# Kernel tuning notes

Hardware: AMD Instinct MI355X
Metric: run time of the kernel (lower is better)

## Reference

```python
import jax, jax.numpy as jnp
import numpy as np

N_LAYER = 6
EPS = 1e-5
THETA = 2.0 ** 16


def _ln(x):
    # LayerNorm without affine params, eps=1e-5 (torch default)
    m = x.mean(-1, keepdims=True)
    v = ((x - m) ** 2).mean(-1, keepdims=True)
    return (x - m) * jax.lax.rsqrt(v + EPS)


def _rope(phases, v):
    # rotate-half over interleaved pairs, phases are in cycles (mod 1 -> radians)
    v_rot = jnp.stack([-v[..., 1::2], v[..., ::2]], axis=-1).reshape(v.shape)
    ph = (phases % 1.0) * (2.0 * jnp.pi)
    return v * jnp.cos(ph) + v_rot * jnp.sin(ph)


def _forward(x, conv_w, conv_b, pos_embed, encoder, encoder_v, decoder, freqs, head_w, head_b):
    B, Cin, H, W = x.shape
    nh, D, N = encoder.shape
    P = conv_w.shape[-1]
    hp, wp = H // P, W // P
    T = hp * wp
    # patch embed: Conv2d(k=P, s=P) == unfold + matmul
    xp = x.reshape(B, Cin, hp, P, wp, P)
    tokens = jnp.einsum('bchpwq,dcpq->bhwd', xp, conv_w).reshape(B, T, D) + conv_b
    h = tokens + pos_embed  # (B, T, D); the unit head dim is handled by einsum broadcasting
    phases = jnp.arange(T, dtype=jnp.float32).reshape(1, 1, T, 1) * freqs  # (1,1,T,N)
    scale = 1.0 / jnp.sqrt(jnp.asarray(N, dtype=x.dtype))
    for _ in range(N_LAYER):  # weights are SHARED across layers, as in the module
        hn = _ln(h)  # (B, T, D)
        x_sparse = jax.nn.relu(jnp.einsum('btd,hdn->bhtn', hn, encoder))  # (B,nh,T,N)
        qr = _rope(phases, x_sparse)
        scores = jax.nn.softmax(jnp.einsum('bhtn,bhsn->bhts', qr, qr) * scale, axis=-1)
        yKV = _ln(jnp.einsum('bhts,bsd->bhtd', scores, hn))  # V = ln'd x, broadcast over heads
        y_sparse = jax.nn.relu(jnp.einsum('bhtd,hdn->bhtn', yKV, encoder_v))
        xy_sparse = x_sparse * y_sparse  # (B,nh,T,N)
        z = xy_sparse.transpose(0, 2, 1, 3).reshape(B, T, nh * N)  # (B,T,nh*N), head-major flatten
        yMLP = _ln(z @ decoder)  # (B,T,D)
        h = _ln(hn + yMLP)
    pooled = _ln(h.mean(axis=1))  # (B,D)
    return pooled @ head_w.T + head_b


def setup_inputs():
    key = jax.random.key(0)
    B, Cin, H, P = 64, 3, 224, 16
    D, nh, mult, ncls = 768, 12, 8, 1000
    N = mult * D // nh  # 512
    T = (H // P) ** 2  # 196
    ks = jax.random.split(key, 7)

    def xav(k, shape, fan_in, fan_out):
        a = (6.0 / (fan_in + fan_out)) ** 0.5
        return jax.random.uniform(k, shape, jnp.float32, -a, a)

    x = jax.random.normal(ks[0], (B, Cin, H, H), jnp.float32)
    conv_w = xav(ks[1], (D, Cin, P, P), Cin * P * P, D)
    conv_b = jnp.zeros((D,), jnp.float32)
    pos_embed = jax.random.normal(ks[2], (1, T, D), jnp.float32) * 0.02
    encoder = xav(ks[3], (nh, D, N), D, N)
    encoder_v = xav(ks[4], (nh, D, N), D, N)
    decoder = xav(ks[5], (nh * N, D), nh * N, D)
    i = jnp.arange(N, dtype=jnp.float32)
    freqs = ((1.0 / THETA) ** ((i // 2) * 2.0 / N)).reshape(1, 1, 1, N)  # paired RoPE freqs
    head_w = xav(ks[6], (ncls, D), D, ncls)
    head_b = jnp.zeros((ncls,), jnp.float32)
    return dict(x=x, conv_w=conv_w, conv_b=conv_b, pos_embed=pos_embed,
                encoder=encoder, encoder_v=encoder_v, decoder=decoder,
                freqs=freqs, head_w=head_w, head_b=head_b)


def reference(x, conv_w, conv_b, pos_embed, encoder, encoder_v, decoder, freqs, head_w, head_b):
    return _forward(x, conv_w, conv_b, pos_embed, encoder, encoder_v, decoder, freqs, head_w, head_b)
```

## Files before the change

### kernel.cpp

```cpp
#include <hip/hip_runtime.h>
#include <hip/hip_bf16.h>


typedef short bf16x8 __attribute__((ext_vector_type(8)));
typedef float f32x4 __attribute__((ext_vector_type(4)));
typedef unsigned short u16;

#define LN_EPS 1e-5f
#define SM_SCALE 0.044194173824159216f
#define TWO_PI 6.283185307179586f
#define MC 3136

typedef __attribute__((address_space(3))) unsigned char* as3p;
typedef const __attribute__((address_space(1))) unsigned char* as1p;

__device__ __forceinline__ void gload16(const u16* g, u16* l) {
    __builtin_amdgcn_global_load_lds((as1p)(const void*)g, (as3p)(void*)l, 16, 0, 0);
}

__device__ __forceinline__ u16 f2bf(float f) {
    __hip_bfloat16 h = __float2bfloat16(f);
    return *reinterpret_cast<u16*>(&h);
}
__device__ __forceinline__ float bf2f(u16 u) {
    return __uint_as_float(((unsigned)u) << 16);
}

__device__ __forceinline__ float block_reduce_sum(float v, float* sm) {
    #pragma unroll
    for (int o = 32; o; o >>= 1) v += __shfl_xor(v, o);
    if ((threadIdx.x & 63) == 0) sm[threadIdx.x >> 6] = v;
    __syncthreads();
    float r = sm[0] + sm[1] + sm[2] + sm[3];
    __syncthreads();
    return r;
}

__device__ __forceinline__ void gemm_core64(const u16* __restrict__ A, int lda,
                                            const u16* __restrict__ Bt, int ldb,
                                            int ksteps, f32x4 acc[4][4],
                                            u16* lds_a, u16* lds_b) {
    const int tid = threadIdx.x;
    const int lane = tid & 63;
    const int wave = tid >> 6;
    const int wr = (wave >> 1) * 64;
    const int wc = (wave & 1) * 64;
    const int lr = lane & 15;
    const int lg = lane >> 4;
    const int rx = lr & 7;
    const int srow = tid >> 3;
    const int gslot = (tid & 7) ^ (srow & 7);
    const u16* ga = A + (long)srow * lda + gslot * 8;
    const u16* gb = Bt + (long)srow * ldb + gslot * 8;
    u16* la = lds_a + tid * 8;
    u16* lb = lds_b + tid * 8;
    for (int k0 = 0; k0 < ksteps; ++k0) {
        __syncthreads();
        #pragma unroll
        for (int j = 0; j < 4; ++j) {
            gload16(ga + (long)(j * 32) * lda, la + j * 2048);
            gload16(gb + (long)(j * 32) * ldb, lb + j * 2048);
        }
        ga += 64; gb += 64;
        __syncthreads();
        bf16x8 af[2][4], bfr[2][4];
        #pragma unroll
        for (int kk = 0; kk < 2; ++kk) {
            const int ps = ((lg + kk * 4) ^ rx) * 8;
            #pragma unroll
            for (int m = 0; m < 4; m++)
                af[kk][m] = *(const bf16x8*)&lds_a[(wr + 16 * m + lr) * 64 + ps];
            #pragma unroll
            for (int n = 0; n < 4; n++)
                bfr[kk][n] = *(const bf16x8*)&lds_b[(wc + 16 * n + lr) * 64 + ps];
        }
        #pragma unroll
        for (int kk = 0; kk < 2; ++kk)
            #pragma unroll
            for (int m = 0; m < 4; m++)
                #pragma unroll
                for (int n = 0; n < 4; n++)
                    acc[m][n] = __builtin_amdgcn_mfma_f32_16x16x32_bf16(
                        af[kk][m], bfr[kk][n], acc[m][n], 0, 0, 0);
    }
}

#define GEMM64_PROLOGUE                                 \
    __shared__ alignas(16) u16 lds_ab[2 * 128 * 64];    \
    u16* lds_a = lds_ab;                                \
    u16* lds_b = lds_ab + 128 * 64;                     \
    f32x4 acc[4][4];                                    \
    _Pragma("unroll")                                   \
    for (int m = 0; m < 4; m++)                         \
        _Pragma("unroll")                               \
        for (int n = 0; n < 4; n++)                     \
            acc[m][n] = (f32x4){0.f, 0.f, 0.f, 0.f};

#define EPI_VARS                                        \
    const int lane = threadIdx.x & 63;                  \
    const int wave = threadIdx.x >> 6;                  \
    const int ewr = (wave >> 1) * 64 + (lane >> 4) * 4; \
    const int ewc = (wave & 1) * 64 + (lane & 15);

__device__ __forceinline__ void gemm_core(const u16* __restrict__ A, int lda,
                                          const u16* __restrict__ Bt, int ldb,
                                          int ksteps, f32x4 acc[4][4],
                                          u16* lds_a, u16* lds_b) {
    const int tid = threadIdx.x;
    const int lane = tid & 63;
    const int wave = tid >> 6;
    const int wr = (wave >> 1) * 64;
    const int wc = (wave & 1) * 64;
    const int lr = lane & 15;
    const int lk = (lane >> 4) * 8;
    const int srow = tid >> 2;
    const int scol = (tid & 3) * 8;
    const u16* ga = A + (long)srow * lda + scol;
    const u16* gb = Bt + (long)srow * ldb + scol;
    const long ha = (long)64 * lda;
    const long hb = (long)64 * ldb;
    u16* la = lds_a + tid * 8;
    u16* lb = lds_b + tid * 8;
    for (int k0 = 0; k0 < ksteps; ++k0) {
        __syncthreads();
        gload16(ga, la);
        gload16(ga + ha, la + 2048);
        gload16(gb, lb);
        gload16(gb + hb, lb + 2048);
        ga += 32; gb += 32;
        __syncthreads();
        bf16x8 af[4], bfr[4];
        #pragma unroll
        for (int m = 0; m < 4; m++)
            af[m] = *(const bf16x8*)&lds_a[(wr + 16 * m + lr) * 32 + lk];
        #pragma unroll
        for (int n = 0; n < 4; n++)
            bfr[n] = *(const bf16x8*)&lds_b[(wc + 16 * n + lr) * 32 + lk];
        #pragma unroll
        for (int m = 0; m < 4; m++)
            #pragma unroll
            for (int n = 0; n < 4; n++)
                acc[m][n] = __builtin_amdgcn_mfma_f32_16x16x32_bf16(af[m], bfr[n], acc[m][n], 0, 0, 0);
    }
}

__global__ __launch_bounds__(256) void k_pack_patches(const float* __restrict__ x,
                                                      u16* __restrict__ ap) {
    int idx = blockIdx.x * 256 + threadIdx.x;
    int r = idx / 768, k = idx - r * 768;
    int b = r / 196, t = r - b * 196;
    int hp = t / 14, wp = t - hp * 14;
    int c = k >> 8, rem = k & 255, p = rem >> 4, q = rem & 15;
    long src = ((long)(b * 3 + c) * 224 + hp * 16 + p) * 224 + wp * 16 + q;
    ap[idx] = f2bf(x[src]);
}

__global__ __launch_bounds__(256) void k_cast(const float* __restrict__ s,
                                              u16* __restrict__ d, int n) {
    int i = blockIdx.x * 256 + threadIdx.x;
    if (i < n) d[i] = f2bf(s[i]);
}

__global__ __launch_bounds__(256) void k_transpose_cast(const float* __restrict__ src,
                                                        u16* __restrict__ dst,
                                                        int R, int C) {
    __shared__ float tile[32][33];
    int c0 = blockIdx.x * 32, r0 = blockIdx.y * 32;
    long base = (long)blockIdx.z * R * C;
    int i = threadIdx.x >> 5, j = threadIdx.x & 31;
    #pragma unroll
    for (int p = 0; p < 4; p++) {
        int rr = i + p * 8;
        tile[rr][j] = src[base + (long)(r0 + rr) * C + c0 + j];
    }
    __syncthreads();
    #pragma unroll
    for (int p = 0; p < 4; p++) {
        int rr = i + p * 8;
        dst[base + (long)(c0 + rr) * R + r0 + j] = f2bf(tile[j][rr]);
    }
}

__global__ __launch_bounds__(256) void k_rope_tab(const float* __restrict__ freqs,
                                                  float* __restrict__ tc,
                                                  float* __restrict__ ts) {
    int idx = blockIdx.x * 256 + threadIdx.x;
    int t = idx >> 9, n = idx & 511;
    float ph = (float)t * freqs[n];
    ph = (ph - floorf(ph)) * TWO_PI;
    tc[idx] = cosf(ph);
    ts[idx] = sinf(ph);
}

__global__ __launch_bounds__(256) void k_colsum(const float* __restrict__ encv,
                                                float* __restrict__ cs) {
    int h = blockIdx.y, c = blockIdx.x * 256 + threadIdx.x;
    const float* base = encv + (long)h * 768 * 512 + c;
    float a = 0.f;
    for (int d = 0; d < 768; d++) a += base[(long)d * 512];
    cs[h * 512 + c] = a;
}

__global__ __launch_bounds__(256) void k_gemm_tokens(const u16* __restrict__ ap,
                                                     const u16* __restrict__ bw,
                                                     const float* __restrict__ cb,
                                                     const float* __restrict__ pe,
                                                     float* __restrict__ hout) {
    GEMM64_PROLOGUE
    int row0 = blockIdx.x * 128, col0 = blockIdx.y * 128;
    gemm_core64(ap + (long)row0 * 768, 768, bw + (long)col0 * 768, 768, 12, acc, lds_a, lds_b);
    EPI_VARS
    const int tid = threadIdx.x;
    float* TF = (float*)lds_ab;
    #pragma unroll
    for (int hf = 0; hf < 2; ++hf) {
        __syncthreads();
        if ((ewr >> 6) == hf) {
            #pragma unroll
            for (int m = 0; m < 4; m++)
                #pragma unroll
                for (int n = 0; n < 4; n++)
                    #pragma unroll
                    for (int i = 0; i < 4; i++) {
                        int row = row0 + ewr + 16 * m + i;
                        int col = col0 + ewc + 16 * n;
                        int t = row % 196;
                        TF[(ewr - hf * 64 + 16 * m + i) * 128 + ewc + 16 * n] =
                            acc[m][n][i] + cb[col] + pe[t * 768 + col];
                    }
        }
        __syncthreads();
        #pragma unroll
        for (int q = 0; q < 8; ++q) {
            int chunk = tid + q * 256;
            int r = chunk >> 5, c = chunk & 31;
            *(f32x4*)&hout[(long)(row0 + hf * 64 + r) * 768 + col0 + c * 4] =
                *(f32x4*)&TF[r * 128 + c * 4];
        }
    }
}

__global__ __launch_bounds__(256) void k_gemm_xs(const u16* __restrict__ hnb,
                                                 const u16* __restrict__ enct,
                                                 const float* __restrict__ tc,
                                                 const float* __restrict__ tsn,
                                                 u16* __restrict__ xs,
                                                 u16* __restrict__ qr) {
    GEMM64_PROLOGUE
    int p = blockIdx.x + 25 * blockIdx.y;
    int w = (p & 7) * 150 + (p >> 3);
    int row0 = (w % 25) * 128, col0 = (w / 25) * 128;
    int head = col0 >> 9, nn0 = col0 & 511;
    gemm_core64(hnb + (long)row0 * 768, 768,
                enct + ((long)head * 512 + nn0) * 768, 768, 12, acc, lds_a, lds_b);
    EPI_VARS
    const int tid = threadIdx.x;
    u16* TU = lds_ab;
    __syncthreads();
    #pragma unroll
    for (int m = 0; m < 4; m++)
        #pragma unroll
        for (int n = 0; n < 4; n++)
            #pragma unroll
            for (int i = 0; i < 4; i++)
                TU[(ewr + 16 * m + i) * 128 + ewc + 16 * n] =
                    f2bf(fmaxf(acc[m][n][i], 0.f));
    __syncthreads();
    #pragma unroll
    for (int q = 0; q < 8; ++q) {
        int chunk = tid + q * 256;
        int r = chunk >> 4, c = chunk & 15;
        int row = row0 + r;
        if (row < MC)
            *(bf16x8*)&xs[((long)head * MC + row) * 512 + nn0 + c * 8] =
                *(bf16x8*)&TU[r * 128 + c * 8];
    }
    __syncthreads();
    #pragma unroll
    for (int m = 0; m < 4; m++)
        #pragma unroll
        for (int n = 0; n < 4; n++)
            #pragma unroll
            for (int i = 0; i < 4; i++) {
                int row = row0 + ewr + 16 * m + i;
                float v = fmaxf(acc[m][n][i], 0.f);
                float pp = __shfl_xor(v, 1);
                if (row < MC) {
                    int t = row % 196;
                    int nn = nn0 + ewc + 16 * n;
                    float cs = tc[t * 512 + nn], sn = tsn[t * 512 + nn];
                    float rot = (nn & 1) ? pp : -pp;
                    TU[(ewr + 16 * m + i) * 128 + ewc + 16 * n] =
                        f2bf(v * cs + rot * sn);
                }
            }
    __syncthreads();
    #pragma unroll
    for (int q = 0; q < 8; ++q) {
        int chunk = tid + q * 256;
        int r = chunk >> 4, c = chunk & 15;
        int row = row0 + r;
        if (row < MC)
            *(bf16x8*)&qr[((long)head * MC + row) * 512 + nn0 + c * 8] =
                *(bf16x8*)&TU[r * 128 + c * 8];
    }
}

__global__ __launch_bounds__(256) void k_attn(const u16* __restrict__ qr,
                                              const u16* __restrict__ hnT,
                                              u16* __restrict__ ykv,
                                              float* __restrict__ stats) {
    __shared__ alignas(16) u16 lds_a[128 * 32];
    __shared__ alignas(16) u16 lds_b[128 * 32];
    __shared__ alignas(16) u16 Pl[128 * 232];
    __shared__ float part[2][128][2];
    const int tid = threadIdx.x, lane = tid & 63, wave = tid >> 6;
    const int wr = (wave >> 1) * 64, wc = (wave & 1) * 64;
    const int lr = lane & 15, lk = (lane >> 4) * 8;
    const int row0 = blockIdx.x * 128, bh = blockIdx.y;
    const int bL = bh & 15;
    const u16* qbase = qr + (long)bh * 196 * 512;

    f32x4 acc0[4][4], acc1[4][4];
    #pragma unroll
    for (int m = 0; m < 4; m++)
        #pragma unroll
        for (int n = 0; n < 4; n++) {
            acc0[m][n] = (f32x4){0.f, 0.f, 0.f, 0.f};
            acc1[m][n] = (f32x4){0.f, 0.f, 0.f, 0.f};
        }
    gemm_core(qbase + (long)row0 * 512, 512, qbase, 512, 16, acc0, lds_a, lds_b);
    gemm_core(qbase + (long)row0 * 512, 512, qbase + 128 * 512, 512, 16, acc1, lds_a, lds_b);

    const int rb = wr + (lane >> 4) * 4;
    #pragma unroll
    for (int m = 0; m < 4; m++)
        #pragma unroll
        for (int i = 0; i < 4; i++) {
            float mx = -1e30f;
            #pragma unroll
            for (int n = 0; n < 4; n++) {
                int c0 = wc + 16 * n + lr;
                if (c0 < 196) mx = fmaxf(mx, acc0[m][n][i]);
                if (c0 + 128 < 196) mx = fmaxf(mx, acc1[m][n][i]);
            }
            #pragma unroll
            for (int o = 1; o < 16; o <<= 1) mx = fmaxf(mx, __shfl_xor(mx, o));
            if (lr == 0) part[0][rb + 16 * m + i][wave & 1] = mx;
        }
    __syncthreads();
    #pragma unroll
    for (int m = 0; m < 4; m++)
        #pragma unroll
        for (int i = 0; i < 4; i++) {
            int row = rb + 16 * m + i;
            float rmx = fmaxf(part[0][row][0], part[0][row][1]);
            float s = 0.f;
            #pragma unroll
            for (int n = 0; n < 4; n++) {
                int c0 = wc + 16 * n + lr;
                float e0 = (c0 < 196) ? __expf((acc0[m][n][i] - rmx) * SM_SCALE) : 0.f;
                float e1 = (c0 + 128 < 196) ? __expf((acc1[m][n][i] - rmx) * SM_SCALE) : 0.f;
                acc0[m][n][i] = e0; acc1[m][n][i] = e1;
                s += e0 + e1;
            }
            #pragma unroll
            for (int o = 1; o < 16; o <<= 1) s += __shfl_xor(s, o);
            if (lr == 0) part[1][row][wave & 1] = s;
        }
    __syncthreads();
    #pragma unroll
    for (int m = 0; m < 4; m++)
        #pragma unroll
        for (int i = 0; i < 4; i++) {
            int row = rb + 16 * m + i;
            float inv = 1.f / (part[1][row][0] + part[1][row][1]);
            #pragma unroll
            for (int n = 0; n < 4; n++) {
                int c0 = wc + 16 * n + lr;
                Pl[row * 232 + c0] = f2bf(acc0[m][n][i] * inv);
                if (c0 + 128 < 224)
                    Pl[row * 232 + c0 + 128] = f2bf(acc1[m][n][i] * inv);
            }
        }
    __syncthreads();
    { float* pf = &part[0][0][0]; pf[tid] = 0.f; pf[tid + 256] = 0.f; }
    const int srow = tid >> 2, scol = (tid & 3) * 8;
    for (int cd = 0; cd < 6; ++cd) {
        const u16* Bt = hnT + ((long)bL * 768 + cd * 128) * 224;
        f32x4 acc[4][4];
        #pragma unroll
        for (int m = 0; m < 4; m++)
            #pragma unroll
            for (int n = 0; n < 4; n++) acc[m][n] = (f32x4){0.f, 0.f, 0.f, 0.f};
        for (int k0 = 0; k0 < 7; ++k0) {
            __syncthreads();
            gload16(Bt + (long)srow * 224 + k0 * 32 + scol, lds_b + tid * 8);
            gload16(Bt + (long)(srow + 64) * 224 + k0 * 32 + scol, lds_b + 2048 + tid * 8);
            __syncthreads();
            bf16x8 af[4], bfr[4];
            #pragma unroll
            for (int m = 0; m < 4; m++)
                af[m] = *(const bf16x8*)&Pl[(wr + 16 * m + lr) * 232 + k0 * 32 + lk];
            #pragma unroll
            for (int n = 0; n < 4; n++)
                bfr[n] = *(const bf16x8*)&lds_b[(wc + 16 * n + lr) * 32 + lk];
            #pragma unroll
            for (int m = 0; m < 4; m++)
                #pragma unroll
                for (int n = 0; n < 4; n++)
                    acc[m][n] = __builtin_amdgcn_mfma_f32_16x16x32_bf16(af[m], bfr[n], acc[m][n], 0, 0, 0);
        }
        #pragma unroll
        for (int m = 0; m < 4; m++)
            #pragma unroll
            for (int i = 0; i < 4; i++) {
                float s = acc[m][0][i] + acc[m][1][i] + acc[m][2][i] + acc[m][3][i];
                float q2 = acc[m][0][i] * acc[m][0][i] + acc[m][1][i] * acc[m][1][i] +
                           acc[m][2][i] * acc[m][2][i] + acc[m][3][i] * acc[m][3][i];
                #pragma unroll
                for (int o = 1; o < 16; o <<= 1) {
                    s += __shfl_xor(s, o);
                    q2 += __shfl_xor(q2, o);
                }
                if (lr == 0) {
                    part[0][rb + 16 * m + i][wave & 1] += s;
                    part[1][rb + 16 * m + i][wave & 1] += q2;
                }
            }
        EPI_VARS
        #pragma unroll
        for (int m = 0; m < 4; m++)
            #pragma unroll
            for (int n = 0; n < 4; n++)
                #pragma unroll
                for (int i = 0; i < 4; i++) {
                    int trow = row0 + ewr + 16 * m + i;
                    if (trow < 196)
                        ykv[((long)bh * 196 + trow) * 768 + cd * 128 + ewc + 16 * n] =
                            f2bf(acc[m][n][i]);
                }
    }
    __syncthreads();
    if (tid < 128) {
        int trow = row0 + tid;
        if (trow < 196) {
            float s = part[0][tid][0] + part[0][tid][1];
            float q2 = part[1][tid][0] + part[1][tid][1];
            float mu = s * (1.f / 768.f);
            float var = q2 * (1.f / 768.f) - mu * mu;
            float2 st;
            st.x = mu;
            st.y = rsqrtf(var + LN_EPS);
            *(float2*)&stats[((long)bh * 196 + trow) * 2] = st;
        }
    }
}

__global__ __launch_bounds__(256) void k_gemm_ys(const u16* __restrict__ ykv,
                                                 const u16* __restrict__ encvt,
                                                 const u16* __restrict__ xs,
                                                 const float* __restrict__ stats,
                                                 const float* __restrict__ colsum,
                                                 u16* __restrict__ z) {
    GEMM64_PROLOGUE
    int p = blockIdx.x + 25 * (blockIdx.y + 4 * blockIdx.z);
    int w = (p & 7) * 150 + (p >> 3);
    int rt = w % 25, rem = w / 25;
    int ct = rem & 3, h = rem >> 2;
    int row0 = rt * 128, col0 = ct * 128;
    gemm_core64(ykv + ((long)h * MC + row0) * 768, 768,
                encvt + ((long)h * 512 + col0) * 768, 768, 12, acc, lds_a, lds_b);
    EPI_VARS
    const int tid = threadIdx.x;
    u16* TU = lds_ab;
    __syncthreads();
    #pragma unroll
    for (int q = 0; q < 8; ++q) {
        int chunk = tid + q * 256;
        int r = chunk >> 4, c = chunk & 15;
        *(bf16x8*)&TU[r * 128 + c * 8] =
            *(const bf16x8*)&xs[((long)h * MC + row0 + r) * 512 + col0 + c * 8];
    }
    __syncthreads();
    #pragma unroll
    for (int m = 0; m < 4; m++)
        #pragma unroll
        for (int i = 0; i < 4; i++) {
            int rloc = ewr + 16 * m + i;
            int row = row0 + rloc;
            float mu = 0.f, rs = 0.f;
            if (row < MC) {
                float2 st = *(const float2*)&stats[((long)h * MC + row) * 2];
                mu = st.x; rs = st.y;
            }
            #pragma unroll
            for (int n = 0; n < 4; n++) {
                int cloc = ewc + 16 * n;
                float cs = colsum[h * 512 + col0 + cloc];
                float v = (acc[m][n][i] - mu * cs) * rs;
                v = fmaxf(v, 0.f) * bf2f(TU[rloc * 128 + cloc]);
                TU[rloc * 128 + cloc] = f2bf(v);
            }
        }
    __syncthreads();
    #pragma unroll
    for (int q = 0; q < 8; ++q) {
        int chunk = tid + q * 256;
        int r = chunk >> 4, c = chunk & 15;
        int row = row0 + r;
        if (row < MC)
            *(bf16x8*)&z[(long)row * 6144 + h * 512 + col0 + c * 8] =
                *(bf16x8*)&TU[r * 128 + c * 8];
    }
}

__global__ __launch_bounds__(256) void k_gemm_mlp(const u16* __restrict__ z,
                                                  const u16* __restrict__ dect,
                                                  float* __restrict__ rawK) {
    GEMM64_PROLOGUE
    int p = blockIdx.x + 25 * (blockIdx.y + 6 * blockIdx.z);
    int w = (p & 7) * 75 + (p >> 3);
    int row0 = (w % 25) * 128, col0 = ((w / 25) % 6) * 128, s = w / 150;
    gemm_core64(z + (long)row0 * 6144 + s * 1536, 6144,
                dect + (long)col0 * 6144 + s * 1536, 6144, 24, acc, lds_a, lds_b);
    EPI_VARS
    const int tid = threadIdx.x;
    float* TF = (float*)lds_ab;
    float* raw = rawK + (long)s * MC * 768;
    #pragma unroll
    for (int hf = 0; hf < 2; ++hf) {
        __syncthreads();
        if ((ewr >> 6) == hf) {
            #pragma unroll
            for (int m = 0; m < 4; m++)
                #pragma unroll
                for (int n = 0; n < 4; n++)
                    #pragma unroll
                    for (int i = 0; i < 4; i++)
                        TF[(ewr - hf * 64 + 16 * m + i) * 128 + ewc + 16 * n] =
                            acc[m][n][i];
        }
        __syncthreads();
        #pragma unroll
        for (int q = 0; q < 8; ++q) {
            int chunk = tid + q * 256;
            int r = chunk >> 5, c = chunk & 31;
            int row = row0 + hf * 64 + r;
            if (row < MC)
                *(f32x4*)&raw[(long)row * 768 + col0 + c * 4] =
                    *(f32x4*)&TF[r * 128 + c * 4];
        }
    }
}

__global__ __launch_bounds__(256) void k_ln1(const float* __restrict__ h,
                                             u16* __restrict__ hnb) {
    __shared__ float sm[4];
    int r = blockIdx.x, tid = threadIdx.x;
    const float* p = h + (long)r * 768;
    float x0 = p[tid], x1 = p[tid + 256], x2 = p[tid + 512];
    float mean = block_reduce_sum(x0 + x1 + x2, sm) * (1.f / 768.f);
    float d0 = x0 - mean, d1 = x1 - mean, d2 = x2 - mean;
    float var = block_reduce_sum(d0 * d0 + d1 * d1 + d2 * d2, sm) * (1.f / 768.f);
    float rs = rsqrtf(var + LN_EPS);
    long ro = (long)r * 768;
    hnb[ro + tid] = f2bf(d0 * rs);
    hnb[ro + tid + 256] = f2bf(d1 * rs);
    hnb[ro + tid + 512] = f2bf(d2 * rs);
}

__global__ __launch_bounds__(256) void k_hnT(const u16* __restrict__ hnb,
                                             u16* __restrict__ hnT) {
    __shared__ u16 tile[32][33];
    int t0 = blockIdx.x * 32, d0 = blockIdx.y * 32, b = blockIdx.z;
    int i = threadIdx.x >> 5, j = threadIdx.x & 31;
    #pragma unroll
    for (int p = 0; p < 4; p++) {
        int t = t0 + i + p * 8;
        tile[i + p * 8][j] = (t < 196) ? hnb[((long)b * 196 + t) * 768 + d0 + j] : (u16)0;
    }
    __syncthreads();
    #pragma unroll
    for (int p = 0; p < 4; p++) {
        int dd = i + p * 8;
        hnT[((long)b * 768 + d0 + dd) * 224 + t0 + j] = tile[j][dd];
    }
}

__global__ __launch_bounds__(256) void k_final_h(const float* __restrict__ rawK,
                                                 u16* __restrict__ hnb) {
    __shared__ float sm[4];
    const long PS = (long)MC * 768;
    int r = blockIdx.x, tid = threadIdx.x;
    const float* rp = rawK + (long)r * 768;
// ... 150 lines not shown
```

Before: 6.880 ms.

## Double-buffer LDS tiles and XOR-swizzle layout in attention kernel GEMMs

Result: slower. 8.286 ms (+20.4%).

```diff
diff --git a/kernel.cpp b/kernel.cpp
--- a/kernel.cpp
+++ b/kernel.cpp
@@ -102,46 +102,55 @@
     const int ewr = (wave >> 1) * 64 + (lane >> 4) * 4; \
     const int ewc = (wave & 1) * 64 + (lane & 15);
 
-__device__ __forceinline__ void gemm_core(const u16* __restrict__ A, int lda,
-                                          const u16* __restrict__ Bt, int ldb,
-                                          int ksteps, f32x4 acc[4][4],
-                                          u16* lds_a, u16* lds_b) {
+__device__ __forceinline__ void gemm_core_sw(const u16* __restrict__ A, int lda,
+                                             const u16* __restrict__ Bt, int ldb,
+                                             int ksteps , f32x4 acc[4][4],
+                                             u16* a0, u16* b0, u16* a1, u16* b1) {
     const int tid = threadIdx.x;
     const int lane = tid & 63;
     const int wave = tid >> 6;
     const int wr = (wave >> 1) * 64;
     const int wc = (wave & 1) * 64;
     const int lr = lane & 15;
-    const int lk = (lane >> 4) * 8;
+    const int lg = lane >> 4;
+    const int ps = (lg ^ ((lr >> 1) & 3)) * 8;
     const int srow = tid >> 2;
-    const int scol = (tid & 3) * 8;
-    const u16* ga = A + (long)srow * lda + scol;
-    const u16* gb = Bt + (long)srow * ldb + scol;
-    const long ha = (long)64 * lda;
-    const long hb = (long)64 * ldb;
-    u16* la = lds_a + tid * 8;
-    u16* lb = lds_b + tid * 8;
-    for (int k0 = 0; k0 < ksteps; ++k0) {
+    const int gslot = (tid & 3) ^ ((srow >> 1) & 3);
+    const u16* ga = A + (long)srow * lda + gslot * 8;
+    const u16* gb = Bt + (long)srow * ldb + gslot * 8;
+    const long ha = (long)64 * lda, hb = (long)64 * ldb;
+
+#define SSTG(pa, pb, k)                                                      \
+    { gload16(ga + (k) * 32, (pa) + tid * 8);                                \
+      gload16(ga + ha + (k) * 32, (pa) + 2048 + tid * 8);                    \
+      gload16(gb + (k) * 32, (pb) + tid * 8);                                \
+      gload16(gb + hb + (k) * 32, (pb) + 2048 + tid * 8); }
+#define SCMP(pa, pb)                                                         \
+    { bf16x8 af[4], bfr[4];                                                  \
+      _Pragma("unroll")                                                      \
+      for (int m = 0; m < 4; m++)                                            \
+          af[m] = *(const bf16x8*)&(pa)[(wr + 16 * m + lr) * 32 + ps];       \
+      _Pragma("unroll")                                                      \
+      for (int n = 0; n < 4; n++)                                            \
+          bfr[n] = *(const bf16x8*)&(pb)[(wc + 16 * n + lr) * 32 + ps];      \
+      _Pragma("unroll")                                                      \
+      for (int m = 0; m < 4; m++)                                            \
+          _Pragma("unroll")                                                  \
+          for (int n = 0; n < 4; n++)                                        \
+              acc[m][n] = __builtin_amdgcn_mfma_f32_16x16x32_bf16(           \
+                  af[m], bfr[n], acc[m][n], 0, 0, 0); }
+
+    SSTG(a0, b0, 0)
+    for (int k0 = 0; k0 < ksteps; k0 += 2) {
         __syncthreads();
-        gload16(ga, la);
-        gload16(ga + ha, la + 2048);
-        gload16(gb, lb);
-        gload16(gb + hb, lb + 2048);
-        ga += 32; gb += 32;
+        if (k0 + 1 < ksteps) SSTG(a1, b1, k0 + 1)
+        SCMP(a0, b0)
         __syncthreads();
-        bf16x8 af[4], bfr[4];
-        #pragma unroll
-        for (int m = 0; m < 4; m++)
-            af[m] = *(const bf16x8*)&lds_a[(wr + 16 * m + lr) * 32 + lk];
-        #pragma unroll
-        for (int n = 0; n < 4; n++)
-            bfr[n] = *(const bf16x8*)&lds_b[(wc + 16 * n + lr) * 32 + lk];
-        #pragma unroll
-        for (int m = 0; m < 4; m++)
-            #pragma unroll
-            for (int n = 0; n < 4; n++)
-                acc[m][n] = __builtin_amdgcn_mfma_f32_16x16x32_bf16(af[m], bfr[n], acc[m][n], 0, 0, 0);
-    }
+        if (k0 + 2 < ksteps) SSTG(a0, b0, k0 + 2)
+        if (k0 + 1 < ksteps) SCMP(a1, b1)
+    }
+#undef SSTG
+#undef SCMP
 }
 
 __global__ __launch_bounds__(256) void k_pack_patches(const float* __restrict__ x,
@@ -316,10 +325,13 @@
     __shared__ float part[2][128][2];
     const int tid = threadIdx.x, lane = tid & 63, wave = tid >> 6;
     const int wr = (wave >> 1) * 64, wc = (wave & 1) * 64;
-    const int lr = lane & 15, lk = (lane >> 4) * 8;
+    const int lr = lane & 15, lg = lane >> 4, lk = lg * 8;
+    const int ps = (lg ^ ((lr >> 1) & 3)) * 8;
     const int row0 = blockIdx.x * 128, bh = blockIdx.y;
     const int bL = bh & 15;
     const u16* qbase = qr + (long)bh * 196 * 512;
+    u16* a1 = Pl;
+    u16* b1 = Pl + 128 * 32;
 
     f32x4 acc0[4][4], acc1[4][4];
     #pragma unroll
@@ -329,8 +341,10 @@
             acc0[m][n] = (f32x4){0.f, 0.f, 0.f, 0.f};
             acc1[m][n] = (f32x4){0.f, 0.f, 0.f, 0.f};
         }
-    gemm_core(qbase + (long)row0 * 512, 512, qbase, 512, 16, acc0, lds_a, lds_b);
-    gemm_core(qbase + (long)row0 * 512, 512, qbase + 128 * 512, 512, 16, acc1, lds_a, lds_b);
+    gemm_core_sw(qbase + (long)row0 * 512, 512, qbase, 512, 16, acc0,
+                 lds_a, lds_b, a1, b1);
+    gemm_core_sw(qbase + (long)row0 * 512, 512, qbase + 128 * 512, 512, 16, acc1,
+                 lds_a, lds_b, a1, b1);
 
     const int rb = wr + (lane >> 4) * 4;
     #pragma unroll
@@ -385,39 +399,51 @@
         }
     __syncthreads();
     { float* pf = &part[0][0][0]; pf[tid] = 0.f; pf[tid + 256] = 0.f; }
-    const int srow = tid >> 2, scol = (tid & 3) * 8;
+    const int srow = tid >> 2;
+    const int gsl = (tid & 3) ^ ((srow >> 1) & 3);
+
+#define PSTG(pb, Btp, k)                                                     \
+    { gload16((Btp) + (long)srow * 224 + (k) * 32 + gsl * 8, (pb) + tid * 8); \
+      gload16((Btp) + (long)(srow + 64) * 224 + (k) * 32 + gsl * 8,          \
+              (pb) + 2048 + tid * 8); }
+#define PCMP(pb, k)                                                          \
+    { bf16x8 af[4], bfr[4];                                                  \
+      _Pragma("unroll")                                                      \
+      for (int m = 0; m < 4; m++)                                            \
+          af[m] = *(const bf16x8*)&Pl[(wr + 16 * m + lr) * 232 + (k) * 32 + lk]; \
+      _Pragma("unroll")                                                      \
+      for (int n = 0; n < 4; n++)                                            \
+          bfr[n] = *(const bf16x8*)&(pb)[(wc + 16 * n + lr) * 32 + ps];      \
+      _Pragma("unroll")                                                      \
+      for (int m = 0; m < 4; m++)                                            \
+          _Pragma("unroll")                                                  \
+          for (int n = 0; n < 4; n++)                                        \
+              pacc[m][n] = __builtin_amdgcn_mfma_f32_16x16x32_bf16(          \
+                  af[m], bfr[n], pacc[m][n], 0, 0, 0); }
+
     for (int cd = 0; cd < 6; ++cd) {
         const u16* Bt = hnT + ((long)bL * 768 + cd * 128) * 224;
-        f32x4 acc[4][4];
+        f32x4 pacc[4][4];
         #pragma unroll
         for (int m = 0; m < 4; m++)
             #pragma unroll
-            for (int n = 0; n < 4; n++) acc[m][n] = (f32x4){0.f, 0.f, 0.f, 0.f};
-        for (int k0 = 0; k0 < 7; ++k0) {
+            for (int n = 0; n < 4; n++) pacc[m][n] = (f32x4){0.f, 0.f, 0.f, 0.f};
+        PSTG(lds_b, Bt, 0)
+        for (int k0 = 0; k0 < 7; k0 += 2) {
             __syncthreads();
-            gload16(Bt + (long)srow * 224 + k0 * 32 + scol, lds_b + tid * 8);
-            gload16(Bt + (long)(srow + 64) * 224 + k0 * 32 + scol, lds_b + 2048 + tid * 8);
+            if (k0 + 1 < 7) PSTG(lds_a, Bt, k0 + 1)
+            PCMP(lds_b, k0)
             __syncthreads();
-            bf16x8 af[4], bfr[4];
-            #pragma unroll
-            for (int m = 0; m < 4; m++)
-                af[m] = *(const bf16x8*)&Pl[(wr + 16 * m + lr) * 232 + k0 * 32 + lk];
-            #pragma unroll
-            for (int n = 0; n < 4; n++)
-                bfr[n] = *(const bf16x8*)&lds_b[(wc + 16 * n + lr) * 32 + lk];
-            #pragma unroll
-            for (int m = 0; m < 4; m++)
-                #pragma unroll
-                for (int n = 0; n < 4; n++)
-                    acc[m][n] = __builtin_amdgcn_mfma_f32_16x16x32_bf16(af[m], bfr[n], acc[m][n], 0, 0, 0);
+            if (k0 + 2 < 7) PSTG(lds_b, Bt, k0 + 2)
+            if (k0 + 1 < 7) PCMP(lds_a, k0 + 1)
         }
         #pragma unroll
         for (int m = 0; m < 4; m++)
             #pragma unroll
             for (int i = 0; i < 4; i++) {
-                float s = acc[m][0][i] + acc[m][1][i] + acc[m][2][i] + acc[m][3][i];
-                float q2 = acc[m][0][i] * acc[m][0][i] + acc[m][1][i] * acc[m][1][i] +
-                           acc[m][2][i] * acc[m][2][i] + acc[m][3][i] * acc[m][3][i];
+                float s = pacc[m][0][i] + pacc[m][1][i] + pacc[m][2][i] + pacc[m][3][i];
+                float q2 = pacc[m][0][i] * pacc[m][0][i] + pacc[m][1][i] * pacc[m][1][i] +
+                           pacc[m][2][i] * pacc[m][2][i] + pacc[m][3][i] * pacc[m][3][i];
                 #pragma unroll
                 for (int o = 1; o < 16; o <<= 1) {
                     s += __shfl_xor(s, o);
@@ -438,9 +464,11 @@
                     int trow = row0 + ewr + 16 * m + i;
                     if (trow < 196)
                         ykv[((long)bh * 196 + trow) * 768 + cd * 128 + ewc + 16 * n] =
-                            f2bf(acc[m][n][i]);
+                            f2bf(pacc[m][n][i]);
                 }
     }
+#undef PSTG
+#undef PCMP
     __syncthreads();
     if (tid < 128) {
         int trow = row0 + tid;
```

## Restructure attention kernel GEMMs with shared A-fragments, wider K-steps and swizzled LDS

Applied to the files above, without the earlier changes.

New measurement: 7.615 ms. +10.7%, slower.

```diff
diff --git a/kernel.cpp b/kernel.cpp
--- a/kernel.cpp
+++ b/kernel.cpp
@@ -102,48 +102,6 @@
     const int ewr = (wave >> 1) * 64 + (lane >> 4) * 4; \
     const int ewc = (wave & 1) * 64 + (lane & 15);
 
-__device__ __forceinline__ void gemm_core(const u16* __restrict__ A, int lda,
-                                          const u16* __restrict__ Bt, int ldb,
-                                          int ksteps, f32x4 acc[4][4],
-                                          u16* lds_a, u16* lds_b) {
-    const int tid = threadIdx.x;
-    const int lane = tid & 63;
-    const int wave = tid >> 6;
-    const int wr = (wave >> 1) * 64;
-    const int wc = (wave & 1) * 64;
-    const int lr = lane & 15;
-    const int lk = (lane >> 4) * 8;
-    const int srow = tid >> 2;
-    const int scol = (tid & 3) * 8;
-    const u16* ga = A + (long)srow * lda + scol;
-    const u16* gb = Bt + (long)srow * ldb + scol;
-    const long ha = (long)64 * lda;
-    const long hb = (long)64 * ldb;
-    u16* la = lds_a + tid * 8;
-    u16* lb = lds_b + tid * 8;
-    for (int k0 = 0; k0 < ksteps; ++k0) {
-        __syncthreads();
-        gload16(ga, la);
-        gload16(ga + ha, la + 2048);
-        gload16(gb, lb);
-        gload16(gb + hb, lb + 2048);
-        ga += 32; gb += 32;
-        __syncthreads();
-        bf16x8 af[4], bfr[4];
-        #pragma unroll
-        for (int m = 0; m < 4; m++)
-            af[m] = *(const bf16x8*)&lds_a[(wr + 16 * m + lr) * 32 + lk];
-        #pragma unroll
-        for (int n = 0; n < 4; n++)
-            bfr[n] = *(const bf16x8*)&lds_b[(wc + 16 * n + lr) * 32 + lk];
-        #pragma unroll
-        for (int m = 0; m < 4; m++)
-            #pragma unroll
-            for (int n = 0; n < 4; n++)
-                acc[m][n] = __builtin_amdgcn_mfma_f32_16x16x32_bf16(af[m], bfr[n], acc[m][n], 0, 0, 0);
-    }
-}
-
 __global__ __launch_bounds__(256) void k_pack_patches(const float* __restrict__ x,
                                                       u16* __restrict__ ap) {
     int idx = blockIdx.x * 256 + threadIdx.x;
@@ -310,16 +268,18 @@
                                               const u16* __restrict__ hnT,
                                               u16* __restrict__ ykv,
                                               float* __restrict__ stats) {
-    __shared__ alignas(16) u16 lds_a[128 * 32];
-    __shared__ alignas(16) u16 lds_b[128 * 32];
+    __shared__ alignas(16) u16 ldsA[128 * 64];
     __shared__ alignas(16) u16 Pl[128 * 232];
     __shared__ float part[2][128][2];
     const int tid = threadIdx.x, lane = tid & 63, wave = tid >> 6;
     const int wr = (wave >> 1) * 64, wc = (wave & 1) * 64;
-    const int lr = lane & 15, lk = (lane >> 4) * 8;
+    const int lr = lane & 15, lg = lane >> 4, lk = lg * 8;
+    const int ewr = wr + lg * 4, ewc = wc + lr;
     const int row0 = blockIdx.x * 128, bh = blockIdx.y;
     const int bL = bh & 15;
     const u16* qbase = qr + (long)bh * 196 * 512;
+    u16* B0 = Pl;
+    u16* B1 = Pl + 128 * 64;
 
     f32x4 acc0[4][4], acc1[4][4];
     #pragma unroll
@@ -329,10 +289,50 @@
             acc0[m][n] = (f32x4){0.f, 0.f, 0.f, 0.f};
             acc1[m][n] = (f32x4){0.f, 0.f, 0.f, 0.f};
         }
-    gemm_core(qbase + (long)row0 * 512, 512, qbase, 512, 16, acc0, lds_a, lds_b);
-    gemm_core(qbase + (long)row0 * 512, 512, qbase + 128 * 512, 512, 16, acc1, lds_a, lds_b);
-
-    const int rb = wr + (lane >> 4) * 4;
+
+    {
+        const int srow = tid >> 3;
+        const int gsl = (tid & 7) ^ (srow & 7);
+        const int rx = lr & 7;
+        const u16* gA = qbase + (long)(row0 + srow) * 512 + gsl * 8;
+        const u16* gB0 = qbase + (long)srow * 512 + gsl * 8;
+        const u16* gB1 = qbase + (long)(128 + srow) * 512 + gsl * 8;
+        for (int k0 = 0; k0 < 8; ++k0) {
+            __syncthreads();
+            #pragma unroll
+            for (int j = 0; j < 4; ++j) {
+                gload16(gA + (long)(32 * j) * 512, ldsA + j * 2048 + tid * 8);
+                gload16(gB0 + (long)(32 * j) * 512, B0 + j * 2048 + tid * 8);
+                gload16(gB1 + (long)(32 * j) * 512, B1 + j * 2048 + tid * 8);
+            }
+            gA += 64; gB0 += 64; gB1 += 64;
+            __syncthreads();
+            #pragma unroll
+            for (int kk = 0; kk < 2; ++kk) {
+                const int ps = ((lg + 4 * kk) ^ rx) * 8;
+                bf16x8 af[4], f0[4], f1[4];
+                #pragma unroll
+                for (int m = 0; m < 4; m++)
+                    af[m] = *(const bf16x8*)&ldsA[(wr + 16 * m + lr) * 64 + ps];
+                #pragma unroll
+                for (int n = 0; n < 4; n++) {
+                    f0[n] = *(const bf16x8*)&B0[(wc + 16 * n + lr) * 64 + ps];
+                    f1[n] = *(const bf16x8*)&B1[(wc + 16 * n + lr) * 64 + ps];
+                }
+                #pragma unroll
+                for (int m = 0; m < 4; m++)
+                    #pragma unroll
+                    for (int n = 0; n < 4; n++) {
+                        acc0[m][n] = __builtin_amdgcn_mfma_f32_16x16x32_bf16(
+                            af[m], f0[n], acc0[m][n], 0, 0, 0);
+                        acc1[m][n] = __builtin_amdgcn_mfma_f32_16x16x32_bf16(
+                            af[m], f1[n], acc1[m][n], 0, 0, 0);
+                    }
+            }
+        }
+    }
+
+    const int rb = wr + lg * 4;
     #pragma unroll
     for (int m = 0; m < 4; m++)
         #pragma unroll
@@ -385,61 +385,82 @@
         }
     __syncthreads();
     { float* pf = &part[0][0][0]; pf[tid] = 0.f; pf[tid + 256] = 0.f; }
-    const int srow = tid >> 2, scol = (tid & 3) * 8;
-    for (int cd = 0; cd < 6; ++cd) {
-        const u16* Bt = hnT + ((long)bL * 768 + cd * 128) * 224;
-        f32x4 acc[4][4];
-        #pragma unroll
-        for (int m = 0; m < 4; m++)
-            #pragma unroll
-            for (int n = 0; n < 4; n++) acc[m][n] = (f32x4){0.f, 0.f, 0.f, 0.f};
-        for (int k0 = 0; k0 < 7; ++k0) {
-            __syncthreads();
-            gload16(Bt + (long)srow * 224 + k0 * 32 + scol, lds_b + tid * 8);
-            gload16(Bt + (long)(srow + 64) * 224 + k0 * 32 + scol, lds_b + 2048 + tid * 8);
-            __syncthreads();
-            bf16x8 af[4], bfr[4];
+
+    {
+        const int srow = tid >> 2;
+        const int gsl = (tid & 3) ^ ((srow >> 1) & 3);
+        const int ps = (lg ^ ((lr >> 1) & 3)) * 8;
+        for (int cp = 0; cp < 3; ++cp) {
+            const u16* Bt0 = hnT + ((long)bL * 768 + (2 * cp) * 128) * 224;
+            const u16* Bt1 = Bt0 + 128 * 224;
+            f32x4 p0[4][4], p1[4][4];
             #pragma unroll
             for (int m = 0; m < 4; m++)
-                af[m] = *(const bf16x8*)&Pl[(wr + 16 * m + lr) * 232 + k0 * 32 + lk];
-            #pragma unroll
-            for (int n = 0; n < 4; n++)
-                bfr[n] = *(const bf16x8*)&lds_b[(wc + 16 * n + lr) * 32 + lk];
+                #pragma unroll
+                for (int n = 0; n < 4; n++) {
+                    p0[m][n] = (f32x4){0.f, 0.f, 0.f, 0.f};
+                    p1[m][n] = (f32x4){0.f, 0.f, 0.f, 0.f};
+                }
+            for (int k0 = 0; k0 < 7; ++k0) {
+                __syncthreads();
+                gload16(Bt0 + (long)srow * 224 + k0 * 32 + gsl * 8, ldsA + tid * 8);
+                gload16(Bt0 + (long)(srow + 64) * 224 + k0 * 32 + gsl * 8, ldsA + 2048 + tid * 8);
+                gload16(Bt1 + (long)srow * 224 + k0 * 32 + gsl * 8, ldsA + 4096 + tid * 8);
+                gload16(Bt1 + (long)(srow + 64) * 224 + k0 * 32 + gsl * 8, ldsA + 6144 + tid * 8);
+                __syncthreads();
+                bf16x8 af[4], f0[4], f1[4];
+                #pragma unroll
+                for (int m = 0; m < 4; m++)
+                    af[m] = *(const bf16x8*)&Pl[(wr + 16 * m + lr) * 232 + k0 * 32 + lk];
+                #pragma unroll
+                for (int n = 0; n < 4; n++) {
+                    f0[n] = *(const bf16x8*)&ldsA[(wc + 16 * n + lr) * 32 + ps];
+                    f1[n] = *(const bf16x8*)&ldsA[4096 + (wc + 16 * n + lr) * 32 + ps];
+                }
+                #pragma unroll
+                for (int m = 0; m < 4; m++)
+                    #pragma unroll
+                    for (int n = 0; n < 4; n++) {
+                        p0[m][n] = __builtin_amdgcn_mfma_f32_16x16x32_bf16(
+                            af[m], f0[n], p0[m][n], 0, 0, 0);
+                        p1[m][n] = __builtin_amdgcn_mfma_f32_16x16x32_bf16(
+                            af[m], f1[n], p1[m][n], 0, 0, 0);
+                    }
+            }
             #pragma unroll
             for (int m = 0; m < 4; m++)
                 #pragma unroll
+                for (int i = 0; i < 4; i++) {
+                    float s = p0[m][0][i] + p0[m][1][i] + p0[m][2][i] + p0[m][3][i]
+                            + p1[m][0][i] + p1[m][1][i] + p1[m][2][i] + p1[m][3][i];
+                    float q2 = p0[m][0][i] * p0[m][0][i] + p0[m][1][i] * p0[m][1][i]
+                             + p0[m][2][i] * p0[m][2][i] + p0[m][3][i] * p0[m][3][i]
+                             + p1[m][0][i] * p1[m][0][i] + p1[m][1][i] * p1[m][1][i]
+                             + p1[m][2][i] * p1[m][2][i] + p1[m][3][i] * p1[m][3][i];
+                    #pragma unroll
+                    for (int o = 1; o < 16; o <<= 1) {
+                        s += __shfl_xor(s, o);
+                        q2 += __shfl_xor(q2, o);
+                    }
+                    if (lr == 0) {
+                        part[0][rb + 16 * m + i][wave & 1] += s;
+                        part[1][rb + 16 * m + i][wave & 1] += q2;
+                    }
+                }
+            #pragma unroll
+            for (int m = 0; m < 4; m++)
+                #pragma unroll
                 for (int n = 0; n < 4; n++)
-                    acc[m][n] = __builtin_amdgcn_mfma_f32_16x16x32_bf16(af[m], bfr[n], acc[m][n], 0, 0, 0);
-        }
-        #pragma unroll
-        for (int m = 0; m < 4; m++)
-            #pragma unroll
-            for (int i = 0; i < 4; i++) {
-                float s = acc[m][0][i] + acc[m][1][i] + acc[m][2][i] + acc[m][3][i];
-                float q2 = acc[m][0][i] * acc[m][0][i] + acc[m][1][i] * acc[m][1][i] +
-                           acc[m][2][i] * acc[m][2][i] + acc[m][3][i] * acc[m][3][i];
-                #pragma unroll
-                for (int o = 1; o < 16; o <<= 1) {
-                    s += __shfl_xor(s, o);
-                    q2 += __shfl_xor(q2, o);
-                }
-                if (lr == 0) {
-                    part[0][rb + 16 * m + i][wave & 1] += s;
-                    part[1][rb + 16 * m + i][wave & 1] += q2;
-                }
-            }
-        EPI_VARS
-        #pragma unroll
-        for (int m = 0; m < 4; m++)
-            #pragma unroll
-            for (int n = 0; n < 4; n++)
-                #pragma unroll
-                for (int i = 0; i < 4; i++) {
-                    int trow = row0 + ewr + 16 * m + i;
-                    if (trow < 196)
-                        ykv[((long)bh * 196 + trow) * 768 + cd * 128 + ewc + 16 * n] =
-                            f2bf(acc[m][n][i]);
-                }
+                    #pragma unroll
+                    for (int i = 0; i < 4; i++) {
+                        int trow = row0 + ewr + 16 * m + i;
+                        if (trow < 196) {
+                            long rbase = ((long)bh * 196 + trow) * 768;
+                            ykv[rbase + (2 * cp) * 128 + ewc + 16 * n] = f2bf(p0[m][n][i]);
+                            ykv[rbase + (2 * cp + 1) * 128 + ewc + 16 * n] = f2bf(p1[m][n][i]);
+                        }
+                    }
+        }
     }
     __syncthreads();
     if (tid < 128) {
```

## Register-prefetch next K tile in GEMM cores and attention, swizzle LDS

Applied to the files above, without the earlier changes.

New measurement: 7.611 ms. +10.6%, slower.

```diff
diff --git a/kernel.cpp b/kernel.cpp
--- a/kernel.cpp
+++ b/kernel.cpp
@@ -10,13 +10,6 @@
 #define SM_SCALE 0.044194173824159216f
 #define TWO_PI 6.283185307179586f
 #define MC 3136
-
-typedef __attribute__((address_space(3))) unsigned char* as3p;
-typedef const __attribute__((address_space(1))) unsigned char* as1p;
-
-__device__ __forceinline__ void gload16(const u16* g, u16* l) {
-    __builtin_amdgcn_global_load_lds((as1p)(const void*)g, (as3p)(void*)l, 16, 0, 0);
-}
 
 __device__ __forceinline__ u16 f2bf(float f) {
     __hip_bfloat16 h = __float2bfloat16(f);
@@ -54,15 +47,28 @@
     const u16* gb = Bt + (long)srow * ldb + gslot * 8;
     u16* la = lds_a + tid * 8;
     u16* lb = lds_b + tid * 8;
+    bf16x8 ra[4], rb[4];
+    #pragma unroll
+    for (int j = 0; j < 4; ++j) {
+        ra[j] = *(const bf16x8*)(ga + (long)(j * 32) * lda);
+        rb[j] = *(const bf16x8*)(gb + (long)(j * 32) * ldb);
+    }
+    ga += 64; gb += 64;
+    #pragma unroll
+    for (int j = 0; j < 4; ++j) {
+        *(bf16x8*)(la + j * 2048) = ra[j];
+        *(bf16x8*)(lb + j * 2048) = rb[j];
+    }
+    __syncthreads();
     for (int k0 = 0; k0 < ksteps; ++k0) {
-        __syncthreads();
-        #pragma unroll
-        for (int j = 0; j < 4; ++j) {
-            gload16(ga + (long)(j * 32) * lda, la + j * 2048);
-            gload16(gb + (long)(j * 32) * ldb, lb + j * 2048);
-        }
-        ga += 64; gb += 64;
-        __syncthreads();
+        if (k0 + 1 < ksteps) {
+            #pragma unroll
+            for (int j = 0; j < 4; ++j) {
+                ra[j] = *(const bf16x8*)(ga + (long)(j * 32) * lda);
+                rb[j] = *(const bf16x8*)(gb + (long)(j * 32) * ldb);
+            }
+            ga += 64; gb += 64;
+        }
         bf16x8 af[2][4], bfr[2][4];
         #pragma unroll
         for (int kk = 0; kk < 2; ++kk) {
@@ -82,6 +88,15 @@
                 for (int n = 0; n < 4; n++)
                     acc[m][n] = __builtin_amdgcn_mfma_f32_16x16x32_bf16(
                         af[kk][m], bfr[kk][n], acc[m][n], 0, 0, 0);
+        __syncthreads();
+        if (k0 + 1 < ksteps) {
+            #pragma unroll
+            for (int j = 0; j < 4; ++j) {
+                *(bf16x8*)(la + j * 2048) = ra[j];
+                *(bf16x8*)(lb + j * 2048) = rb[j];
+            }
+        }
+        __syncthreads();
     }
 }
 
@@ -102,45 +117,57 @@
     const int ewr = (wave >> 1) * 64 + (lane >> 4) * 4; \
     const int ewc = (wave & 1) * 64 + (lane & 15);
 
-__device__ __forceinline__ void gemm_core(const u16* __restrict__ A, int lda,
-                                          const u16* __restrict__ Bt, int ldb,
-                                          int ksteps, f32x4 acc[4][4],
-                                          u16* lds_a, u16* lds_b) {
+__device__ __forceinline__ void gemm_core32r(const u16* __restrict__ A, int lda,
+                                             const u16* __restrict__ Bt, int ldb,
+                                             int ksteps, f32x4 acc[4][4],
+                                             u16* lds_a, u16* lds_b) {
     const int tid = threadIdx.x;
     const int lane = tid & 63;
     const int wave = tid >> 6;
     const int wr = (wave >> 1) * 64;
     const int wc = (wave & 1) * 64;
     const int lr = lane & 15;
-    const int lk = (lane >> 4) * 8;
+    const int lg = lane >> 4;
+    const int ps = (lg ^ ((lr >> 1) & 3)) * 8;
     const int srow = tid >> 2;
-    const int scol = (tid & 3) * 8;
-    const u16* ga = A + (long)srow * lda + scol;
-    const u16* gb = Bt + (long)srow * ldb + scol;
-    const long ha = (long)64 * lda;
-    const long hb = (long)64 * ldb;
+    const int gslot = (tid & 3) ^ ((srow >> 1) & 3);
+    const u16* ga = A + (long)srow * lda + gslot * 8;
+    const u16* gb = Bt + (long)srow * ldb + gslot * 8;
+    const long ha = (long)64 * lda, hb = (long)64 * ldb;
     u16* la = lds_a + tid * 8;
     u16* lb = lds_b + tid * 8;
+    bf16x8 r0, r1, r2, r3;
+    r0 = *(const bf16x8*)(ga); r1 = *(const bf16x8*)(ga + ha);
+    r2 = *(const bf16x8*)(gb); r3 = *(const bf16x8*)(gb + hb);
+    ga += 32; gb += 32;
+    *(bf16x8*)la = r0; *(bf16x8*)(la + 2048) = r1;
+    *(bf16x8*)lb = r2; *(bf16x8*)(lb + 2048) = r3;
+    __syncthreads();
     for (int k0 = 0; k0 < ksteps; ++k0) {
-        __syncthreads();
-        gload16(ga, la);
-        gload16(ga + ha, la + 2048);
-        gload16(gb, lb);
-        gload16(gb + hb, lb + 2048);
-        ga += 32; gb += 32;
-        __syncthreads();
+        if (k0 + 1 < ksteps) {
+            r0 = *(const bf16x8*)(ga); r1 = *(const bf16x8*)(ga + ha);
+            r2 = *(const bf16x8*)(gb); r3 = *(const bf16x8*)(gb + hb);
+            ga += 32; gb += 32;
+        }
         bf16x8 af[4], bfr[4];
         #pragma unroll
         for (int m = 0; m < 4; m++)
-            af[m] = *(const bf16x8*)&lds_a[(wr + 16 * m + lr) * 32 + lk];
+            af[m] = *(const bf16x8*)&lds_a[(wr + 16 * m + lr) * 32 + ps];
         #pragma unroll
         for (int n = 0; n < 4; n++)
-            bfr[n] = *(const bf16x8*)&lds_b[(wc + 16 * n + lr) * 32 + lk];
+            bfr[n] = *(const bf16x8*)&lds_b[(wc + 16 * n + lr) * 32 + ps];
         #pragma unroll
         for (int m = 0; m < 4; m++)
             #pragma unroll
             for (int n = 0; n < 4; n++)
-                acc[m][n] = __builtin_amdgcn_mfma_f32_16x16x32_bf16(af[m], bfr[n], acc[m][n], 0, 0, 0);
+                acc[m][n] = __builtin_amdgcn_mfma_f32_16x16x32_bf16(
+                    af[m], bfr[n], acc[m][n], 0, 0, 0);
+        __syncthreads();
+        if (k0 + 1 < ksteps) {
+            *(bf16x8*)la = r0; *(bf16x8*)(la + 2048) = r1;
+            *(bf16x8*)lb = r2; *(bf16x8*)(lb + 2048) = r3;
+        }
+        __syncthreads();
     }
 }
 
@@ -316,7 +343,8 @@
     __shared__ float part[2][128][2];
     const int tid = threadIdx.x, lane = tid & 63, wave = tid >> 6;
     const int wr = (wave >> 1) * 64, wc = (wave & 1) * 64;
-    const int lr = lane & 15, lk = (lane >> 4) * 8;
+    const int lr = lane & 15, lg = lane >> 4, lk = lg * 8;
+    const int ps = (lg ^ ((lr >> 1) & 3)) * 8;
     const int row0 = blockIdx.x * 128, bh = blockIdx.y;
     const int bL = bh & 15;
     const u16* qbase = qr + (long)bh * 196 * 512;
@@ -329,10 +357,10 @@
             acc0[m][n] = (f32x4){0.f, 0.f, 0.f, 0.f};
             acc1[m][n] = (f32x4){0.f, 0.f, 0.f, 0.f};
         }
-    gemm_core(qbase + (long)row0 * 512, 512, qbase, 512, 16, acc0, lds_a, lds_b);
-    gemm_core(qbase + (long)row0 * 512, 512, qbase + 128 * 512, 512, 16, acc1, lds_a, lds_b);
-
-    const int rb = wr + (lane >> 4) * 4;
+    gemm_core32r(qbase + (long)row0 * 512, 512, qbase, 512, 16, acc0, lds_a, lds_b);
+    gemm_core32r(qbase + (long)row0 * 512, 512, qbase + 128 * 512, 512, 16, acc1, lds_a, lds_b);
+
+    const int rb = wr + lg * 4;
     #pragma unroll
     for (int m = 0; m < 4; m++)
         #pragma unroll
@@ -385,39 +413,55 @@
         }
     __syncthreads();
     { float* pf = &part[0][0][0]; pf[tid] = 0.f; pf[tid + 256] = 0.f; }
-    const int srow = tid >> 2, scol = (tid & 3) * 8;
+    const int srow = tid >> 2;
+    const int gsl = (tid & 3) ^ ((srow >> 1) & 3);
+    const int ewr2 = wr + lg * 4, ewc2 = wc + lr;
     for (int cd = 0; cd < 6; ++cd) {
         const u16* Bt = hnT + ((long)bL * 768 + cd * 128) * 224;
-        f32x4 acc[4][4];
+        const u16* gb = Bt + (long)srow * 224 + gsl * 8;
+        f32x4 pacc[4][4];
         #pragma unroll
         for (int m = 0; m < 4; m++)
             #pragma unroll
-            for (int n = 0; n < 4; n++) acc[m][n] = (f32x4){0.f, 0.f, 0.f, 0.f};
+            for (int n = 0; n < 4; n++) pacc[m][n] = (f32x4){0.f, 0.f, 0.f, 0.f};
+        bf16x8 r0 = *(const bf16x8*)(gb);
+        bf16x8 r1 = *(const bf16x8*)(gb + (long)64 * 224);
+        __syncthreads();
+        *(bf16x8*)(lds_b + tid * 8) = r0;
+        *(bf16x8*)(lds_b + 2048 + tid * 8) = r1;
+        __syncthreads();
         for (int k0 = 0; k0 < 7; ++k0) {
-            __syncthreads();
-            gload16(Bt + (long)srow * 224 + k0 * 32 + scol, lds_b + tid * 8);
-            gload16(Bt + (long)(srow + 64) * 224 + k0 * 32 + scol, lds_b + 2048 + tid * 8);
-            __syncthreads();
+            if (k0 < 6) {
+                r0 = *(const bf16x8*)(gb + (k0 + 1) * 32);
+                r1 = *(const bf16x8*)(gb + (long)64 * 224 + (k0 + 1) * 32);
+            }
             bf16x8 af[4], bfr[4];
             #pragma unroll
             for (int m = 0; m < 4; m++)
                 af[m] = *(const bf16x8*)&Pl[(wr + 16 * m + lr) * 232 + k0 * 32 + lk];
             #pragma unroll
             for (int n = 0; n < 4; n++)
-                bfr[n] = *(const bf16x8*)&lds_b[(wc + 16 * n + lr) * 32 + lk];
+                bfr[n] = *(const bf16x8*)&lds_b[(wc + 16 * n + lr) * 32 + ps];
             #pragma unroll
             for (int m = 0; m < 4; m++)
                 #pragma unroll
                 for (int n = 0; n < 4; n++)
-                    acc[m][n] = __builtin_amdgcn_mfma_f32_16x16x32_bf16(af[m], bfr[n], acc[m][n], 0, 0, 0);
+                    pacc[m][n] = __builtin_amdgcn_mfma_f32_16x16x32_bf16(
+                        af[m], bfr[n], pacc[m][n], 0, 0, 0);
+            __syncthreads();
+            if (k0 < 6) {
+                *(bf16x8*)(lds_b + tid * 8) = r0;
+                *(bf16x8*)(lds_b + 2048 + tid * 8) = r1;
+            }
+            __syncthreads();
         }
         #pragma unroll
         for (int m = 0; m < 4; m++)
             #pragma unroll
             for (int i = 0; i < 4; i++) {
-                float s = acc[m][0][i] + acc[m][1][i] + acc[m][2][i] + acc[m][3][i];
-                float q2 = acc[m][0][i] * acc[m][0][i] + acc[m][1][i] * acc[m][1][i] +
-                           acc[m][2][i] * acc[m][2][i] + acc[m][3][i] * acc[m][3][i];
+                float s = pacc[m][0][i] + pacc[m][1][i] + pacc[m][2][i] + pacc[m][3][i];
+                float q2 = pacc[m][0][i] * pacc[m][0][i] + pacc[m][1][i] * pacc[m][1][i] +
+                           pacc[m][2][i] * pacc[m][2][i] + pacc[m][3][i] * pacc[m][3][i];
                 #pragma unroll
                 for (int o = 1; o < 16; o <<= 1) {
                     s += __shfl_xor(s, o);
@@ -428,17 +472,16 @@
                     part[1][rb + 16 * m + i][wave & 1] += q2;
                 }
             }
-        EPI_VARS
         #pragma unroll
         for (int m = 0; m < 4; m++)
             #pragma unroll
             for (int n = 0; n < 4; n++)
                 #pragma unroll
                 for (int i = 0; i < 4; i++) {
-                    int trow = row0 + ewr + 16 * m + i;
+                    int trow = row0 + ewr2 + 16 * m + i;
                     if (trow < 196)
-                        ykv[((long)bh * 196 + trow) * 768 + cd * 128 + ewc + 16 * n] =
-                            f2bf(acc[m][n][i]);
+                        ykv[((long)bh * 196 + trow) * 768 + cd * 128 + ewc2 + 16 * n] =
+                            f2bf(pacc[m][n][i]);
                 }
     }
     __syncthreads();
```
